# Optimization experiments

Hardware: AMD Instinct MI355X
Metric: run time of the kernel (lower is better)

The kernel has to match this reference:

```python
import jax, jax.numpy as jnp
import numpy as np

FFT_LEN = 256
BATCH = 65536


def _dft_kernels():
    n = np.arange(FFT_LEN)
    k = n.reshape(-1, 1)
    cos_k = np.cos(2 * np.pi * k * n / FFT_LEN).astype(np.float32)   # [K, N]
    sin_k = (-np.sin(2 * np.pi * k * n / FFT_LEN)).astype(np.float32)  # [K, N], note the minus sign
    return jnp.asarray(cos_k), jnp.asarray(sin_k)


def setup_inputs() -> dict:
    key = jax.random.key(0)
    x = jax.random.normal(key, (BATCH, 2, FFT_LEN), dtype=jnp.float32)
    cos_kernel, sin_kernel = _dft_kernels()
    return {"x": x, "cos_kernel": cos_kernel, "sin_kernel": sin_kernel}


def reference(x, cos_kernel, sin_kernel):
    # x: [B, 2, 256] -> real/imag channels. Conv1d(kernel=256, no pad) over L=256
    # is exactly a dense 256x256 matmul per channel (a direct O(n^2) DFT).
    x_real = x[:, 0, :]  # [B, 256]
    x_imag = x[:, 1, :]  # [B, 256]
    # real_conv(v) = cos_kernel @ v ; imag_conv(v) = sin_kernel @ v
    real_part = jnp.einsum('kn,bn->bk', cos_kernel, x_real) - jnp.einsum('kn,bn->bk', sin_kernel, x_imag)
    imag_part = jnp.einsum('kn,bn->bk', cos_kernel, x_imag) + jnp.einsum('kn,bn->bk', sin_kernel, x_real)
    out = jnp.concatenate([real_part, imag_part], axis=1)  # [B, 512]
    return out[:, :, None]  # [B, 512, 1] matches torch conv output length 1
```

## Files before the change

### kernel.cpp

```cpp
#include <hip/hip_runtime.h>
#include <hip/hip_bf16.h>
#include <stdint.h>


typedef __attribute__((ext_vector_type(8))) short bf16x8;
typedef __attribute__((ext_vector_type(4))) float f32x4;

#define KDIM 512
#define NDIM 512
#define BM 64

__device__ __forceinline__ ushort f2bf(float f) {
  union { float f; uint32_t u; } v; v.f = f;
  uint32_t r = (v.u + 0x7fffu + ((v.u >> 16) & 1u)) >> 16;
  return (ushort)r;
}

__global__ __launch_bounds__(512) void build_w_kernel(const float* __restrict__ cosk,
                                                      const float* __restrict__ sink,
                                                      ushort* __restrict__ Wf) {
  int g = blockIdx.x * 512 + threadIdx.x;
  int lane = g & 63;
  int nt = (g >> 6) & 31;
  int j = nt * 16 + (lane & 15);
  int kbase = (g >> 11) * 32 + (lane >> 4) * 8;
  bf16x8 w8;
#pragma unroll
  for (int e = 0; e < 8; ++e) {
    int k = kbase + e;
    float v;
    if (j < 256) {
      v = (k < 256) ? cosk[(j << 8) + k] : -sink[(j << 8) + (k - 256)];
    } else {
      int jj = j - 256;
      v = (k < 256) ? sink[(jj << 8) + k] : cosk[(jj << 8) + (k - 256)];
    }
    w8[e] = (short)f2bf(v);
  }
  *reinterpret_cast<bf16x8*>(Wf + (size_t)g * 8) = w8;
}

__device__ __forceinline__ bf16x8 cvt8(f32x4 a, f32x4 b) {
  bf16x8 w8;
  w8[0] = (short)f2bf(a[0]); w8[1] = (short)f2bf(a[1]);
  w8[2] = (short)f2bf(a[2]); w8[3] = (short)f2bf(a[3]);
  w8[4] = (short)f2bf(b[0]); w8[5] = (short)f2bf(b[1]);
  w8[6] = (short)f2bf(b[2]); w8[7] = (short)f2bf(b[3]);
  return w8;
}

__global__ __launch_bounds__(512) void dft_gemm_kernel(const float* __restrict__ A,
                                                       const ushort* __restrict__ Wf,
                                                       float* __restrict__ out) {
  __shared__ ushort As[2][BM * 64];

  const int tid  = threadIdx.x;
  const int lane = tid & 63;
  const int wid  = tid >> 6;
  const int m0   = blockIdx.x * BM;
  const int c0   = wid * 64;

  const int srow = tid >> 3;
  const int skq  = (tid & 7) * 8;
  const float* ap = A + (size_t)(m0 + srow) * KDIM + skq;
  const int swidx = (srow << 6) + (skq ^ ((srow & 7) << 3));

  const int lrow = lane & 15;
  const int lk8  = (lane >> 4) * 8;

  const ushort* wp = Wf + (size_t)(c0 >> 4) * 512 + lane * 8;

  f32x4 acc[4][4] = {};

  f32x4 q0 = *reinterpret_cast<const f32x4*>(ap);
  f32x4 q1 = *reinterpret_cast<const f32x4*>(ap + 4);
  f32x4 p0 = *reinterpret_cast<const f32x4*>(ap + 64);
  f32x4 p1 = *reinterpret_cast<const f32x4*>(ap + 68);
  *reinterpret_cast<bf16x8*>(&As[0][swidx]) = cvt8(q0, q1);
  asm volatile("s_waitcnt lgkmcnt(0)" ::: "memory");
  __builtin_amdgcn_s_barrier();

#pragma unroll
  for (int t = 0; t < 8; ++t) {
    if (t < 7)
      *reinterpret_cast<bf16x8*>(&As[(t + 1) & 1][swidx]) = cvt8(p0, p1);

    bf16x8 wfr[2][4];
#pragma unroll
    for (int kk = 0; kk < 2; ++kk)
#pragma unroll
      for (int mi = 0; mi < 4; ++mi)
        wfr[kk][mi] = *reinterpret_cast<const bf16x8*>(
            wp + (size_t)((t * 2 + kk) * 32 + mi) * 512);

    if (t < 6) {
      p0 = *reinterpret_cast<const f32x4*>(ap + (t + 2) * 64);
      p1 = *reinterpret_cast<const f32x4*>(ap + (t + 2) * 64 + 4);
    }

#pragma unroll
    for (int kk = 0; kk < 2; ++kk) {
      bf16x8 xfr[4];
#pragma unroll
      for (int ni = 0; ni < 4; ++ni) {
        int row = ni * 16 + lrow;
        int idx = (row << 6) + ((kk * 32 + lk8) ^ ((lrow & 7) << 3));
        xfr[ni] = *reinterpret_cast<const bf16x8*>(&As[t & 1][idx]);
      }
#pragma unroll
      for (int mi = 0; mi < 4; ++mi)
#pragma unroll
        for (int ni = 0; ni < 4; ++ni)
          acc[mi][ni] = __builtin_amdgcn_mfma_f32_16x16x32_bf16(
              wfr[kk][mi], xfr[ni], acc[mi][ni], 0, 0, 0);
    }

    if (t < 7) {
      asm volatile("s_waitcnt lgkmcnt(0)" ::: "memory");
      __builtin_amdgcn_s_barrier();
    }
  }

  const int jbase = c0 + (lane >> 4) * 4;
#pragma unroll
  for (int ni = 0; ni < 4; ++ni) {
    size_t rowb = (size_t)(m0 + ni * 16 + lrow) * NDIM;
#pragma unroll
    for (int mi = 0; mi < 4; ++mi) {
      f32x4* op = reinterpret_cast<f32x4*>(out + rowb + jbase + mi * 16);
      __builtin_nontemporal_store(acc[mi][ni], op);
    }
  }
}

extern "C" void kernel_launch(void* const* d_in, const int* in_sizes, int n_in,
                              void* d_out, int out_size, void* d_ws, size_t ws_size,
                              hipStream_t stream) {
  const float* x    = (const float*)d_in[0];
  const float* cosk = (const float*)d_in[1];
  const float* sink = (const float*)d_in[2];
  float* out = (float*)d_out;
  ushort* Wf = (ushort*)d_ws;

  build_w_kernel<<<64, 512, 0, stream>>>(cosk, sink, Wf);
  dft_gemm_kernel<<<65536 / BM, 512, 0, stream>>>(x, Wf, out);
}
```

Measured before the change: 73.47 us.

## Drop LDS staging; load X straight into registers with 3-deep prefetch

The GEMM no longer stages X in shared memory. Each wave now loads its fp32 X fragments directly from global memory into registers, using a 3-slot register ring to prefetch, so the LDS round trip and the per-step barriers go away. The tile is reshaped to 64 rows by 128 output columns per 256-thread block, and block IDs are remapped so that the four column blocks sharing an X tile land on the same XCD and can reuse it in L2. The bf16 conversion now uses the packed v_cvt_pk_bf16_f32 instruction, and the nontemporal stores are replaced by plain stores. In exchange, each X row is read from global or L2 four times instead of once, and register pressure rises from holding the ring.

```diff
diff --git a/kernel.cpp b/kernel.cpp
--- a/kernel.cpp
+++ b/kernel.cpp
@@ -8,7 +8,6 @@
 
 #define KDIM 512
 #define NDIM 512
-#define BM 64
 
 __device__ __forceinline__ ushort f2bf(float f) {
   union { float f; uint32_t u; } v; v.f = f;
@@ -41,95 +40,89 @@
 }
 
 __device__ __forceinline__ bf16x8 cvt8(f32x4 a, f32x4 b) {
-  bf16x8 w8;
-  w8[0] = (short)f2bf(a[0]); w8[1] = (short)f2bf(a[1]);
-  w8[2] = (short)f2bf(a[2]); w8[3] = (short)f2bf(a[3]);
-  w8[4] = (short)f2bf(b[0]); w8[5] = (short)f2bf(b[1]);
-  w8[6] = (short)f2bf(b[2]); w8[7] = (short)f2bf(b[3]);
-  return w8;
+  uint32_t r0, r1, r2, r3;
+  asm("v_cvt_pk_bf16_f32 %0, %1, %2" : "=v"(r0) : "v"(a[0]), "v"(a[1]));
+  asm("v_cvt_pk_bf16_f32 %0, %1, %2" : "=v"(r1) : "v"(a[2]), "v"(a[3]));
+  asm("v_cvt_pk_bf16_f32 %0, %1, %2" : "=v"(r2) : "v"(b[0]), "v"(b[1]));
+  asm("v_cvt_pk_bf16_f32 %0, %1, %2" : "=v"(r3) : "v"(b[2]), "v"(b[3]));
+  union { uint32_t u[4]; bf16x8 v; } u;
+  u.u[0] = r0; u.u[1] = r1; u.u[2] = r2; u.u[3] = r3;
+  return u.v;
 }
 
-__global__ __launch_bounds__(512) void dft_gemm_kernel(const float* __restrict__ A,
-                                                       const ushort* __restrict__ Wf,
-                                                       float* __restrict__ out) {
-  __shared__ ushort As[2][BM * 64];
-
+__global__ __launch_bounds__(256, 2) void dft_gemm_kernel(const float* __restrict__ A,
+                                                          const ushort* __restrict__ Wf,
+                                                          float* __restrict__ out) {
   const int tid  = threadIdx.x;
   const int lane = tid & 63;
   const int wid  = tid >> 6;
-  const int m0   = blockIdx.x * BM;
-  const int c0   = wid * 64;
+  const int bid  = blockIdx.x;
+  const int xcd  = bid & 7;
+  const int i    = bid >> 3;
+  const int s    = (i >> 2) * 8 + xcd;
+  const int jb   = i & 3;
+  const int m0   = s * 64;
+  const int c0   = jb * 128 + wid * 32;
+  const int lrow = lane & 15;
+  const int g16  = lane >> 4;
 
-  const int srow = tid >> 3;
-  const int skq  = (tid & 7) * 8;
-  const float* ap = A + (size_t)(m0 + srow) * KDIM + skq;
-  const int swidx = (srow << 6) + (skq ^ ((srow & 7) << 3));
-
-  const int lrow = lane & 15;
-  const int lk8  = (lane >> 4) * 8;
-
+  const float* xp0 = A + (size_t)(m0 + lrow) * KDIM + g16 * 8;
   const ushort* wp = Wf + (size_t)(c0 >> 4) * 512 + lane * 8;
 
-  f32x4 acc[4][4] = {};
-
-  f32x4 q0 = *reinterpret_cast<const f32x4*>(ap);
-  f32x4 q1 = *reinterpret_cast<const f32x4*>(ap + 4);
-  f32x4 p0 = *reinterpret_cast<const f32x4*>(ap + 64);
-  f32x4 p1 = *reinterpret_cast<const f32x4*>(ap + 68);
-  *reinterpret_cast<bf16x8*>(&As[0][swidx]) = cvt8(q0, q1);
-  asm volatile("s_waitcnt lgkmcnt(0)" ::: "memory");
-  __builtin_amdgcn_s_barrier();
+  f32x4 acc[2][4] = {};
+  f32x4 xq[3][8];
+  bf16x8 wq[3][2];
 
 #pragma unroll
-  for (int t = 0; t < 8; ++t) {
-    if (t < 7)
-      *reinterpret_cast<bf16x8*>(&As[(t + 1) & 1][swidx]) = cvt8(p0, p1);
+  for (int p = 0; p < 3; ++p) {
+#pragma unroll
+    for (int ni = 0; ni < 4; ++ni) {
+      const float* q = xp0 + (size_t)ni * 16 * KDIM + p * 32;
+      xq[p][2 * ni]     = *reinterpret_cast<const f32x4*>(q);
+      xq[p][2 * ni + 1] = *reinterpret_cast<const f32x4*>(q + 4);
+    }
+    wq[p][0] = *reinterpret_cast<const bf16x8*>(wp + (size_t)(p * 32)     * 512);
+    wq[p][1] = *reinterpret_cast<const bf16x8*>(wp + (size_t)(p * 32 + 1) * 512);
+  }
 
-    bf16x8 wfr[2][4];
 #pragma unroll
-    for (int kk = 0; kk < 2; ++kk)
+  for (int t = 0; t < 16; ++t) {
+    const int sl = t % 3;
+
+    bf16x8 xf[4];
 #pragma unroll
-      for (int mi = 0; mi < 4; ++mi)
-        wfr[kk][mi] = *reinterpret_cast<const bf16x8*>(
-            wp + (size_t)((t * 2 + kk) * 32 + mi) * 512);
+    for (int ni = 0; ni < 4; ++ni)
+      xf[ni] = cvt8(xq[sl][2 * ni], xq[sl][2 * ni + 1]);
 
-    if (t < 6) {
-      p0 = *reinterpret_cast<const f32x4*>(ap + (t + 2) * 64);
-      p1 = *reinterpret_cast<const f32x4*>(ap + (t + 2) * 64 + 4);
+    if (t < 13) {
+#pragma unroll
+      for (int ni = 0; ni < 4; ++ni) {
+        const float* q = xp0 + (size_t)ni * 16 * KDIM + (t + 3) * 32;
+        xq[sl][2 * ni]     = *reinterpret_cast<const f32x4*>(q);
+        xq[sl][2 * ni + 1] = *reinterpret_cast<const f32x4*>(q + 4);
+      }
     }
 
 #pragma unroll
-    for (int kk = 0; kk < 2; ++kk) {
-      bf16x8 xfr[4];
-#pragma unroll
-      for (int ni = 0; ni < 4; ++ni) {
-        int row = ni * 16 + lrow;
-        int idx = (row << 6) + ((kk * 32 + lk8) ^ ((lrow & 7) << 3));
-        xfr[ni] = *reinterpret_cast<const bf16x8*>(&As[t & 1][idx]);
-      }
-#pragma unroll
-      for (int mi = 0; mi < 4; ++mi)
-#pragma unroll
-        for (int ni = 0; ni < 4; ++ni)
-          acc[mi][ni] = __builtin_amdgcn_mfma_f32_16x16x32_bf16(
-              wfr[kk][mi], xfr[ni], acc[mi][ni], 0, 0, 0);
+    for (int ni = 0; ni < 4; ++ni) {
+      acc[0][ni] = __builtin_amdgcn_mfma_f32_16x16x32_bf16(
+          wq[sl][0], xf[ni], acc[0][ni], 0, 0, 0);
+      acc[1][ni] = __builtin_amdgcn_mfma_f32_16x16x32_bf16(
+          wq[sl][1], xf[ni], acc[1][ni], 0, 0, 0);
     }
 
-    if (t < 7) {
-      asm volatile("s_waitcnt lgkmcnt(0)" ::: "memory");
-      __builtin_amdgcn_s_barrier();
+    if (t < 13) {
+      wq[sl][0] = *reinterpret_cast<const bf16x8*>(wp + (size_t)((t + 3) * 32)     * 512);
+      wq[sl][1] = *reinterpret_cast<const bf16x8*>(wp + (size_t)((t + 3) * 32 + 1) * 512);
     }
   }
 
-  const int jbase = c0 + (lane >> 4) * 4;
+  const int jbase = c0 + g16 * 4;
 #pragma unroll
   for (int ni = 0; ni < 4; ++ni) {
     size_t rowb = (size_t)(m0 + ni * 16 + lrow) * NDIM;
-#pragma unroll
-    for (int mi = 0; mi < 4; ++mi) {
-      f32x4* op = reinterpret_cast<f32x4*>(out + rowb + jbase + mi * 16);
-      __builtin_nontemporal_store(acc[mi][ni], op);
-    }
+    *reinterpret_cast<f32x4*>(out + rowb + jbase)      = acc[0][ni];
+    *reinterpret_cast<f32x4*>(out + rowb + jbase + 16) = acc[1][ni];
   }
 }
 
@@ -143,5 +136,5 @@
   ushort* Wf = (ushort*)d_ws;
 
   build_w_kernel<<<64, 512, 0, stream>>>(cosk, sink, Wf);
-  dft_gemm_kernel<<<65536 / BM, 512, 0, stream>>>(x, Wf, out);
+  dft_gemm_kernel<<<4096, 256, 0, stream>>>(x, Wf, out);
 }
```

Measured after the change: 274.1 us. +273.0%, slower.
